# Performance work log

Hardware: AMD Instinct MI355X
Metric: run time of the kernel (lower is better)

Reference implementation:

```python
import jax, jax.numpy as jnp
import numpy as np

N_NODES = 50000   # n_nodes (adjacency is [N,N])
NNZ = 800000      # nonzeros per support (avg degree 16)
S = 3             # number of supports
D_IN = 512
D_OUT = 256


def setup_inputs() -> dict:
    key = jax.random.key(0)
    k0, k1, k2, k3, k4, k5 = jax.random.split(key, 6)
    x = jax.random.normal(k0, (N_NODES, D_IN), dtype=jnp.float32)
    # glorot-uniform per-support weights, stacked [S, D_IN, D_OUT]
    scale = float(np.sqrt(6.0 / (D_IN + D_OUT)))
    W = jax.random.uniform(k1, (S, D_IN, D_OUT), dtype=jnp.float32, minval=-scale, maxval=scale)
    rows = jax.random.randint(k2, (S, NNZ), 0, N_NODES, dtype=jnp.int32)
    cols = jax.random.randint(k3, (S, NNZ), 0, N_NODES, dtype=jnp.int32)
    vals = jax.random.uniform(k4, (S, NNZ), dtype=jnp.float32)
    # Conv1d(in=S, out=1, k=1, bias=False) == learned weighted sum over supports
    cw = jax.random.normal(k5, (S,), dtype=jnp.float32) * 0.5
    return {"x": x, "W": W, "rows": rows, "cols": cols, "vals": vals, "cw": cw}


def reference(x, W, rows, cols, vals, cw):
    # mod='output': out = relu( sum_i cw[i] * (A_i @ (x @ W_i)) )
    def spmm(r, c, v, pre):
        # A in COO: out[r] += v * pre[c]
        msgs = v[:, None] * pre[c]          # [NNZ, D_OUT] gather
        return jax.ops.segment_sum(msgs, r, num_segments=N_NODES)

    out = jnp.zeros((N_NODES, D_OUT), dtype=x.dtype)
    for i in range(S):                      # small fixed support count
        pre = x @ W[i]                      # dense GEMM [N, D_OUT]
        out = out + cw[i] * spmm(rows[i], cols[i], vals[i], pre)
    return jax.nn.relu(out)
```

## Files before the change

### kernel.cpp

```cpp
#include <hip/hip_runtime.h>
#include <stdint.h>

#define N_NODES 50000
#define NNZ     800000
#define SUP     3
#define D_IN    512
#define D_OUT   256
#define TOT_E   (SUP * NNZ)
#define NBUCK   196
#define CAP     13312
#define CHUNK   10240

typedef __attribute__((ext_vector_type(8))) short bf16x8;
typedef __attribute__((ext_vector_type(4))) float f32x4;

static __device__ __forceinline__ unsigned short f2bf(float f) {
    unsigned int u = __float_as_uint(f);
    unsigned int r = (u + 0x7fffu + ((u >> 16) & 1u)) >> 16;
    return (unsigned short)r;
}
static __device__ __forceinline__ unsigned int pack_bf2(float lo, float hi) {
    unsigned int a = __float_as_uint(lo) + 0x8000u;
    unsigned int b = __float_as_uint(hi) + 0x8000u;
    return (a >> 16) | (b & 0xffff0000u);
}
static __device__ __forceinline__ float bf2f(unsigned short h) {
    return __uint_as_float(((unsigned int)h) << 16);
}

__global__ void wprep_kernel(const float* __restrict__ W, unsigned short* __restrict__ Wt) {
    int idx = blockIdx.x * 256 + threadIdx.x;
    if (idx >= SUP * D_IN * D_OUT) return;
    int n = idx & (D_OUT - 1);
    int k = (idx >> 8) & (D_IN - 1);
    int s = idx >> 17;
    Wt[((size_t)s * D_OUT + n) * D_IN + k] = f2bf(W[idx]);
}

__global__ __launch_bounds__(256) void bucket_kernel(const int* __restrict__ rows,
                                                     const int* __restrict__ cols,
                                                     const float* __restrict__ vals,
                                                     const float* __restrict__ cw,
                                                     int* __restrict__ bucket_cursor,
                                                     int2* __restrict__ buck) {
    __shared__ int hist[NBUCK];
    __shared__ int sc[256];
    __shared__ int sstart[NBUCK];
    __shared__ int lcur[NBUCK];
    __shared__ int gbase[NBUCK];
    __shared__ unsigned char bucket_of[CHUNK];
    __shared__ int2 stage[CHUNK];

    const int tid = threadIdx.x;
    const int base_n = blockIdx.x * CHUNK;
    const int count = min(CHUNK, TOT_E - base_n);
    float cw0 = cw[0], cw1 = cw[1], cw2 = cw[2];

    for (int i = tid; i < NBUCK; i += 256) hist[i] = 0;
    __syncthreads();
    for (int i = tid; i < count; i += 256) {
        atomicAdd(&hist[rows[base_n + i] >> 8], 1);
    }
    __syncthreads();
    sc[tid] = (tid < NBUCK) ? hist[tid] : 0;
    __syncthreads();
    for (int off = 1; off < 256; off <<= 1) {
        int t = (tid >= off) ? sc[tid - off] : 0;
        __syncthreads();
        sc[tid] += t;
        __syncthreads();
    }
    if (tid < NBUCK) {
        int st = sc[tid] - hist[tid];
        sstart[tid] = st;
        lcur[tid]   = st;
        gbase[tid]  = atomicAdd(&bucket_cursor[tid], hist[tid]);
    }
    __syncthreads();
    for (int i = tid; i < count; i += 256) {
        int n = base_n + i;
        int r = rows[n];
        int c = cols[n];
        float v = vals[n];
        int s = n / NNZ;
        float w = v * (s == 0 ? cw0 : (s == 1 ? cw1 : cw2));
        int b = r >> 8;
        int p = atomicAdd(&lcur[b], 1);
        stage[p] = make_int2(((r & 255) << 18) | (s * N_NODES + c), __float_as_int(w));
        bucket_of[p] = (unsigned char)b;
    }
    __syncthreads();
    for (int i = tid; i < count; i += 256) {
        int b = bucket_of[i];
        int local_off = i - sstart[b];
        buck[(size_t)b * CAP + gbase[b] + local_off] = stage[i];
    }
}

__global__ __launch_bounds__(256) void sort_kernel(const int2* __restrict__ buck,
                                                   const int* __restrict__ bucket_cursor,
                                                   int2* __restrict__ cv,
                                                   int* __restrict__ base,
                                                   int* __restrict__ cnt) {
    __shared__ int hist[256];
    __shared__ int sc[256];
    __shared__ int sstart[256];
    __shared__ int cur[256];
    __shared__ int2 stage[CAP];

    const int b = blockIdx.x;
    const int tid = threadIdx.x;
    const int sz = bucket_cursor[b];
    const int2* src = buck + (size_t)b * CAP;

    hist[tid] = 0;
    __syncthreads();
    for (int i = tid; i < sz; i += 256) {
        atomicAdd(&hist[((unsigned)src[i].x) >> 18], 1);
    }
    __syncthreads();
    sc[tid] = hist[tid];
    __syncthreads();
    for (int off = 1; off < 256; off <<= 1) {
        int t = (tid >= off) ? sc[tid - off] : 0;
        __syncthreads();
        sc[tid] += t;
        __syncthreads();
    }
    int st = sc[tid] - hist[tid];
    sstart[tid] = st;
    cur[tid] = st;
    __syncthreads();
    for (int i = tid; i < sz; i += 256) {
        int2 e = src[i];
        int rl = ((unsigned)e.x) >> 18;
        int p = atomicAdd(&cur[rl], 1);
        stage[p] = make_int2(e.x & 0x3FFFF, e.y);
    }
    __syncthreads();
    size_t gb = (size_t)b * CAP;
    for (int i = tid; i < sz; i += 256) cv[gb + i] = stage[i];
    int r = b * 256 + tid;
    if (r < N_NODES) {
        base[r] = (int)gb + sstart[tid];
        cnt[r]  = hist[tid];
    }
}

__global__ __launch_bounds__(256) void gemm_kernel(const float* __restrict__ x,
                                                   const unsigned short* __restrict__ Wt,
                                                   unsigned short* __restrict__ pre) {
    __shared__ unsigned short lds_a[128 * 40];
    __shared__ unsigned short lds_b[128 * 40];
    const int m0 = blockIdx.x * 128;
    const int n0 = blockIdx.y * 128;
    const int s  = blockIdx.z;
    const unsigned short* wt = Wt + (size_t)s * D_OUT * D_IN;
    const int tid  = threadIdx.x;
    const int wave = tid >> 6;
    const int lane = tid & 63;
    const int quad = lane >> 4;
    const int lo   = lane & 15;
    const int wm = (wave & 1) * 64;
    const int wn = (wave >> 1) * 64;

    f32x4 acc[4][4] = {};

    const int ar = tid >> 1;
    const int ac = (tid & 1) * 16;
    const int gm = m0 + ar;
    const float* xrow = x + (size_t)gm * D_IN;
    const unsigned short* wrow = wt + (size_t)(n0 + ar) * D_IN;

    for (int kb = 0; kb < D_IN; kb += 32) {
        unsigned int aw[8];
        if (gm < N_NODES) {
            float4 f0 = *(const float4*)(xrow + kb + ac);
            float4 f1 = *(const float4*)(xrow + kb + ac + 4);
            float4 f2 = *(const float4*)(xrow + kb + ac + 8);
            float4 f3 = *(const float4*)(xrow + kb + ac + 12);
            aw[0] = pack_bf2(f0.x, f0.y); aw[1] = pack_bf2(f0.z, f0.w);
            aw[2] = pack_bf2(f1.x, f1.y); aw[3] = pack_bf2(f1.z, f1.w);
            aw[4] = pack_bf2(f2.x, f2.y); aw[5] = pack_bf2(f2.z, f2.w);
            aw[6] = pack_bf2(f3.x, f3.y); aw[7] = pack_bf2(f3.z, f3.w);
        } else {
            #pragma unroll
            for (int q = 0; q < 8; ++q) aw[q] = 0;
        }
        uint4 b0 = *(const uint4*)(wrow + kb + ac);
        uint4 b1 = *(const uint4*)(wrow + kb + ac + 8);

        __syncthreads();
        *(uint4*)&lds_a[ar * 40 + ac]     = make_uint4(aw[0], aw[1], aw[2], aw[3]);
        *(uint4*)&lds_a[ar * 40 + ac + 8] = make_uint4(aw[4], aw[5], aw[6], aw[7]);
        *(uint4*)&lds_b[ar * 40 + ac]     = b0;
        *(uint4*)&lds_b[ar * 40 + ac + 8] = b1;
        __syncthreads();

        bf16x8 af[4], bfr[4];
        #pragma unroll
        for (int i = 0; i < 4; ++i)
            af[i] = *(const bf16x8*)&lds_a[(wm + 16 * i + lo) * 40 + quad * 8];
        #pragma unroll
        for (int j = 0; j < 4; ++j)
            bfr[j] = *(const bf16x8*)&lds_b[(wn + 16 * j + lo) * 40 + quad * 8];
        #pragma unroll
        for (int i = 0; i < 4; ++i)
            #pragma unroll
            for (int j = 0; j < 4; ++j)
                acc[i][j] = __builtin_amdgcn_mfma_f32_16x16x32_bf16(af[i], bfr[j], acc[i][j], 0, 0, 0);
    }

    #pragma unroll
    for (int i = 0; i < 4; ++i) {
        #pragma unroll
        for (int j = 0; j < 4; ++j) {
            int gn = n0 + wn + 16 * j + lo;
            #pragma unroll
            for (int r = 0; r < 4; ++r) {
                int gm2 = m0 + wm + 16 * i + quad * 4 + r;
                if (gm2 < N_NODES)
                    pre[((size_t)s * N_NODES + gm2) * D_OUT + gn] = f2bf(acc[i][j][r]);
            }
        }
    }
}

__global__ __launch_bounds__(256) void spmm_kernel(const unsigned short* __restrict__ pre,
                                                   const int* __restrict__ base,
                                                   const int* __restrict__ cnt,
                                                   const int2* __restrict__ cv,
                                                   float* __restrict__ out) {
    int row  = blockIdx.x * 4 + (threadIdx.x >> 6);
    int lane = threadIdx.x & 63;
    int start = base[row];
    int end   = start + cnt[row];
    float a0 = 0.f, a1 = 0.f, a2 = 0.f, a3 = 0.f;
    int j = start;
    for (; j + 4 <= end; j += 4) {
        int2 e0 = cv[j + 0];
        int2 e1 = cv[j + 1];
        int2 e2 = cv[j + 2];
        int2 e3 = cv[j + 3];
        ushort4 p0 = *(const ushort4*)(pre + (size_t)e0.x * D_OUT + lane * 4);
        ushort4 p1 = *(const ushort4*)(pre + (size_t)e1.x * D_OUT + lane * 4);
        ushort4 p2 = *(const ushort4*)(pre + (size_t)e2.x * D_OUT + lane * 4);
        ushort4 p3 = *(const ushort4*)(pre + (size_t)e3.x * D_OUT + lane * 4);
        float w0 = __int_as_float(e0.y), w1 = __int_as_float(e1.y);
        float w2 = __int_as_float(e2.y), w3 = __int_as_float(e3.y);
        a0 += w0 * bf2f(p0.x) + w1 * bf2f(p1.x) + w2 * bf2f(p2.x) + w3 * bf2f(p3.x);
        a1 += w0 * bf2f(p0.y) + w1 * bf2f(p1.y) + w2 * bf2f(p2.y) + w3 * bf2f(p3.y);
        a2 += w0 * bf2f(p0.z) + w1 * bf2f(p1.z) + w2 * bf2f(p2.z) + w3 * bf2f(p3.z);
        a3 += w0 * bf2f(p0.w) + w1 * bf2f(p1.w) + w2 * bf2f(p2.w) + w3 * bf2f(p3.w);
    }
    for (; j < end; ++j) {
        int2 e = cv[j];
        float w = __int_as_float(e.y);
        ushort4 p = *(const ushort4*)(pre + (size_t)e.x * D_OUT + lane * 4);
        a0 += w * bf2f(p.x);
        a1 += w * bf2f(p.y);
        a2 += w * bf2f(p.z);
        a3 += w * bf2f(p.w);
    }
    float4 o = make_float4(fmaxf(a0, 0.f), fmaxf(a1, 0.f), fmaxf(a2, 0.f), fmaxf(a3, 0.f));
    *(float4*)(out + (size_t)row * D_OUT + lane * 4) = o;
}

extern "C" void kernel_launch(void* const* d_in, const int* in_sizes, int n_in,
                              void* d_out, int out_size, void* d_ws, size_t ws_size,
                              hipStream_t stream) {
    const float* x    = (const float*)d_in[0];
    const float* W    = (const float*)d_in[1];
    const int*   rows = (const int*)d_in[2];
    const int*   cols = (const int*)d_in[3];
    const float* vals = (const float*)d_in[4];
    const float* cw   = (const float*)d_in[5];
    float* out = (float*)d_out;

    char* ws = (char*)d_ws;
    size_t off = 0;
    auto alloc = [&](size_t bytes) -> void* {
        void* p = ws + off;
        off += (bytes + 255) & ~(size_t)255;
        return p;
    };
    unsigned short* pre  = (unsigned short*)alloc((size_t)SUP * N_NODES * D_OUT * 2);
    unsigned short* Wt   = (unsigned short*)alloc((size_t)SUP * D_OUT * D_IN * 2);
    int* base            = (int*)alloc((size_t)N_NODES * 4);
    int* cnt             = (int*)alloc((size_t)N_NODES * 4);
    int* bucket_cursor   = (int*)alloc((size_t)NBUCK * 4);
    int2* cv             = (int2*)alloc((size_t)NBUCK * CAP * 8);
    int2* buck           = (int2*)pre;

    hipMemsetAsync(bucket_cursor, 0, (size_t)NBUCK * 4, stream);

    bucket_kernel<<<(TOT_E + CHUNK - 1) / CHUNK, 256, 0, stream>>>(rows, cols, vals, cw,
                                                                   bucket_cursor, buck);
    sort_kernel<<<NBUCK, 256, 0, stream>>>(buck, bucket_cursor, cv, base, cnt);
    wprep_kernel<<<(SUP * D_IN * D_OUT + 255) / 256, 256, 0, stream>>>(W, Wt);
    gemm_kernel<<<dim3((N_NODES + 127) / 128, D_OUT / 128, SUP), 256, 0, stream>>>(x, Wt, pre);
    spmm_kernel<<<N_NODES / 4, 256, 0, stream>>>(pre, base, cnt, cv, out);
}
```

Measured before the change: 516.3 us.

## Halve row-bucket size, reorder GEMM grid for x reuse, deepen SpMM unroll

Row buckets now cover 128 rows instead of 256. That doubles the bucket count and shrinks the chunk and capacity sizes, giving more sort blocks with smaller LDS staging. The GEMM grid is remapped so the six (support, column-tile) blocks that read the same x row tile are launched next to each other, improving L2 reuse of x. The SpMM loop gains an 8-edge unrolled stage to put more gather loads in flight. In exchange, the sort kernel leaves half its threads idle during the scan, and the smaller per-bucket capacity carries some overflow risk.

Result: no change. 517.2 us (+0.2%).

```diff
diff --git a/kernel.cpp b/kernel.cpp
--- a/kernel.cpp
+++ b/kernel.cpp
@@ -7,9 +7,9 @@
 #define D_IN    512
 #define D_OUT   256
 #define TOT_E   (SUP * NNZ)
-#define NBUCK   196
-#define CAP     13312
-#define CHUNK   10240
+#define NBUCK   391
+#define CAP     6976
+#define CHUNK   6144
 
 typedef __attribute__((ext_vector_type(8))) short bf16x8;
 typedef __attribute__((ext_vector_type(4))) float f32x4;
@@ -48,7 +48,7 @@
     __shared__ int sstart[NBUCK];
     __shared__ int lcur[NBUCK];
     __shared__ int gbase[NBUCK];
-    __shared__ unsigned char bucket_of[CHUNK];
+    __shared__ unsigned short bucket_of[CHUNK];
     __shared__ int2 stage[CHUNK];
 
     const int tid = threadIdx.x;
@@ -59,10 +59,13 @@
     for (int i = tid; i < NBUCK; i += 256) hist[i] = 0;
     __syncthreads();
     for (int i = tid; i < count; i += 256) {
-        atomicAdd(&hist[rows[base_n + i] >> 8], 1);
-    }
-    __syncthreads();
-    sc[tid] = (tid < NBUCK) ? hist[tid] : 0;
+        atomicAdd(&hist[rows[base_n + i] >> 7], 1);
+    }
+    __syncthreads();
+    int b0 = 2 * tid, b1 = b0 + 1;
+    int h0 = (b0 < NBUCK) ? hist[b0] : 0;
+    int h1 = (b1 < NBUCK) ? hist[b1] : 0;
+    sc[tid] = h0 + h1;
     __syncthreads();
     for (int off = 1; off < 256; off <<= 1) {
         int t = (tid >= off) ? sc[tid - off] : 0;
@@ -70,12 +73,11 @@
         sc[tid] += t;
         __syncthreads();
     }
-    if (tid < NBUCK) {
-        int st = sc[tid] - hist[tid];
-        sstart[tid] = st;
-        lcur[tid]   = st;
-        gbase[tid]  = atomicAdd(&bucket_cursor[tid], hist[tid]);
-    }
+    int excl = sc[tid] - (h0 + h1);
+    if (b0 < NBUCK) { sstart[b0] = excl;      lcur[b0] = excl; }
+    if (b1 < NBUCK) { sstart[b1] = excl + h0; lcur[b1] = excl + h0; }
+    for (int i = tid; i < NBUCK; i += 256)
+        gbase[i] = atomicAdd(&bucket_cursor[i], hist[i]);
     __syncthreads();
     for (int i = tid; i < count; i += 256) {
         int n = base_n + i;
@@ -84,10 +86,10 @@
         float v = vals[n];
         int s = n / NNZ;
         float w = v * (s == 0 ? cw0 : (s == 1 ? cw1 : cw2));
-        int b = r >> 8;
+        int b = r >> 7;
         int p = atomicAdd(&lcur[b], 1);
-        stage[p] = make_int2(((r & 255) << 18) | (s * N_NODES + c), __float_as_int(w));
-        bucket_of[p] = (unsigned char)b;
+        stage[p] = make_int2(((r & 127) << 18) | (s * N_NODES + c), __float_as_int(w));
+        bucket_of[p] = (unsigned short)b;
     }
     __syncthreads();
     for (int i = tid; i < count; i += 256) {
@@ -102,10 +104,10 @@
                                                    int2* __restrict__ cv,
                                                    int* __restrict__ base,
                                                    int* __restrict__ cnt) {
-    __shared__ int hist[256];
-    __shared__ int sc[256];
-    __shared__ int sstart[256];
-    __shared__ int cur[256];
+    __shared__ int hist[128];
+    __shared__ int sc[128];
+    __shared__ int sstart[128];
+    __shared__ int cur[128];
     __shared__ int2 stage[CAP];
 
     const int b = blockIdx.x;
@@ -113,23 +115,25 @@
     const int sz = bucket_cursor[b];
     const int2* src = buck + (size_t)b * CAP;
 
-    hist[tid] = 0;
+    if (tid < 128) hist[tid] = 0;
     __syncthreads();
     for (int i = tid; i < sz; i += 256) {
         atomicAdd(&hist[((unsigned)src[i].x) >> 18], 1);
     }
     __syncthreads();
-    sc[tid] = hist[tid];
-    __syncthreads();
-    for (int off = 1; off < 256; off <<= 1) {
-        int t = (tid >= off) ? sc[tid - off] : 0;
-        __syncthreads();
-        sc[tid] += t;
-        __syncthreads();
-    }
-    int st = sc[tid] - hist[tid];
-    sstart[tid] = st;
-    cur[tid] = st;
+    if (tid < 128) sc[tid] = hist[tid];
+    __syncthreads();
+    for (int off = 1; off < 128; off <<= 1) {
+        int t = (tid >= off && tid < 128) ? sc[tid - off] : 0;
+        __syncthreads();
+        if (tid < 128) sc[tid] += t;
+        __syncthreads();
+    }
+    if (tid < 128) {
+        int st = sc[tid] - hist[tid];
+        sstart[tid] = st;
+        cur[tid] = st;
+    }
     __syncthreads();
     for (int i = tid; i < sz; i += 256) {
         int2 e = src[i];
@@ -140,8 +144,8 @@
     __syncthreads();
     size_t gb = (size_t)b * CAP;
     for (int i = tid; i < sz; i += 256) cv[gb + i] = stage[i];
-    int r = b * 256 + tid;
-    if (r < N_NODES) {
+    int r = b * 128 + tid;
+    if (tid < 128 && r < N_NODES) {
         base[r] = (int)gb + sstart[tid];
         cnt[r]  = hist[tid];
     }
@@ -152,9 +156,9 @@
                                                    unsigned short* __restrict__ pre) {
     __shared__ unsigned short lds_a[128 * 40];
     __shared__ unsigned short lds_b[128 * 40];
-    const int m0 = blockIdx.x * 128;
-    const int n0 = blockIdx.y * 128;
-    const int s  = blockIdx.z;
+    const int m0 = blockIdx.y * 128;
+    const int n0 = (blockIdx.x & 1) * 128;
+    const int s  = blockIdx.x >> 1;
     const unsigned short* wt = Wt + (size_t)s * D_OUT * D_IN;
     const int tid  = threadIdx.x;
     const int wave = tid >> 6;
@@ -237,21 +241,39 @@
     int end   = start + cnt[row];
     float a0 = 0.f, a1 = 0.f, a2 = 0.f, a3 = 0.f;
     int j = start;
+    for (; j + 8 <= end; j += 8) {
+        int2 e[8];
+        #pragma unroll
+        for (int q = 0; q < 8; ++q) e[q] = cv[j + q];
+        ushort4 p[8];
+        #pragma unroll
+        for (int q = 0; q < 8; ++q)
+            p[q] = *(const ushort4*)(pre + (size_t)e[q].x * D_OUT + lane * 4);
+        #pragma unroll
+        for (int q = 0; q < 8; ++q) {
+            float w = __int_as_float(e[q].y);
+            a0 += w * bf2f(p[q].x);
+            a1 += w * bf2f(p[q].y);
+            a2 += w * bf2f(p[q].z);
+            a3 += w * bf2f(p[q].w);
+        }
+    }
     for (; j + 4 <= end; j += 4) {
-        int2 e0 = cv[j + 0];
-        int2 e1 = cv[j + 1];
-        int2 e2 = cv[j + 2];
-        int2 e3 = cv[j + 3];
-        ushort4 p0 = *(const ushort4*)(pre + (size_t)e0.x * D_OUT + lane * 4);
-        ushort4 p1 = *(const ushort4*)(pre + (size_t)e1.x * D_OUT + lane * 4);
-        ushort4 p2 = *(const ushort4*)(pre + (size_t)e2.x * D_OUT + lane * 4);
-        ushort4 p3 = *(const ushort4*)(pre + (size_t)e3.x * D_OUT + lane * 4);
-        float w0 = __int_as_float(e0.y), w1 = __int_as_float(e1.y);
-        float w2 = __int_as_float(e2.y), w3 = __int_as_float(e3.y);
-        a0 += w0 * bf2f(p0.x) + w1 * bf2f(p1.x) + w2 * bf2f(p2.x) + w3 * bf2f(p3.x);
-        a1 += w0 * bf2f(p0.y) + w1 * bf2f(p1.y) + w2 * bf2f(p2.y) + w3 * bf2f(p3.y);
-        a2 += w0 * bf2f(p0.z) + w1 * bf2f(p1.z) + w2 * bf2f(p2.z) + w3 * bf2f(p3.z);
-        a3 += w0 * bf2f(p0.w) + w1 * bf2f(p1.w) + w2 * bf2f(p2.w) + w3 * bf2f(p3.w);
+        int2 e[4];
+        #pragma unroll
+        for (int q = 0; q < 4; ++q) e[q] = cv[j + q];
+        ushort4 p[4];
+        #pragma unroll
+        for (int q = 0; q < 4; ++q)
+            p[q] = *(const ushort4*)(pre + (size_t)e[q].x * D_OUT + lane * 4);
+        #pragma unroll
+        for (int q = 0; q < 4; ++q) {
+            float w = __int_as_float(e[q].y);
+            a0 += w * bf2f(p[q].x);
+            a1 += w * bf2f(p[q].y);
+            a2 += w * bf2f(p[q].z);
+            a3 += w * bf2f(p[q].w);
+        }
     }
     for (; j < end; ++j) {
         int2 e = cv[j];
@@ -298,6 +320,6 @@
                                                                    bucket_cursor, buck);
     sort_kernel<<<NBUCK, 256, 0, stream>>>(buck, bucket_cursor, cv, base, cnt);
     wprep_kernel<<<(SUP * D_IN * D_OUT + 255) / 256, 256, 0, stream>>>(W, Wt);
-    gemm_kernel<<<dim3((N_NODES + 127) / 128, D_OUT / 128, SUP), 256, 0, stream>>>(x, Wt, pre);
+    gemm_kernel<<<dim3(6, 391), 256, 0, stream>>>(x, Wt, pre);
     spmm_kernel<<<N_NODES / 4, 256, 0, stream>>>(pre, base, cnt, cv, out);
 }
```
